# Kernel optimization log

Measured on AMD Instinct MI355X. Metric: run time of the kernel, lower is better.

Reference implementation:

```python
import jax, jax.numpy as jnp
import numpy as np

N_NODES = 50000


def gcn_conv(x, src, dst, W, b):
    """PyG GCNConv: symmetric-normalized aggregation with self-loops.
    out[i] = sum_{j->i} deg^{-1/2}[j] deg^{-1/2}[i] (x_j @ W) + b
    src/dst already include self-loop edges.
    """
    n = x.shape[0]
    ew = jnp.ones(src.shape[0], dtype=x.dtype)
    deg = jax.ops.segment_sum(ew, dst, num_segments=n)  # [N]
    dinv = jnp.where(deg > 0, jax.lax.rsqrt(deg), 0.0).astype(x.dtype)
    norm = dinv[src] * dinv[dst]  # [E+N]
    xw = x @ W  # [N, z] dense transform first (as PyG does)
    msg = xw[src] * norm[:, None]  # gather + scale, [E+N, z]
    out = jax.ops.segment_sum(msg, dst, num_segments=n)  # scatter-add
    return out + b


def prelu(x, a):
    return jnp.where(x > 0, x, a * x)


def setup_inputs() -> dict:
    key = jax.random.key(0)
    k1, k2, k3, k4 = jax.random.split(key, 4)
    in_dim = z_dim = 96
    n_edges = 800000
    x = jax.random.normal(k1, (N_NODES, in_dim), dtype=jnp.float32)
    edge_index = jax.random.randint(k2, (2, n_edges), 0, N_NODES, dtype=jnp.int32)
    # Glorot-style init for GCN weights
    s1 = 1.0 / np.sqrt(in_dim)
    W1 = jax.random.uniform(k3, (in_dim, z_dim), jnp.float32, -s1, s1)
    W2 = jax.random.uniform(k4, (z_dim, z_dim), jnp.float32, -s1, s1)
    b1 = jnp.zeros((z_dim,), jnp.float32)
    b2 = jnp.zeros((z_dim,), jnp.float32)
    prelu_a = jnp.full((z_dim,), 0.25, jnp.float32)  # shared PReLU, per-channel
    return {"x": x, "edge_index": edge_index, "W1": W1, "b1": b1,
            "W2": W2, "b2": b2, "prelu_a": prelu_a}


def reference(x, edge_index, W1, b1, W2, b2, prelu_a):
    n = x.shape[0]
    loop = jnp.arange(n, dtype=edge_index.dtype)
    src = jnp.concatenate([edge_index[0], loop])
    dst = jnp.concatenate([edge_index[1], loop])
    h = prelu(gcn_conv(x, src, dst, W1, b1), prelu_a)
    h = prelu(gcn_conv(h, src, dst, W2, b2), prelu_a)
    return h
```

## Files before the change

### kernel.cpp

```cpp
#include <hip/hip_runtime.h>
#include <hip/hip_fp16.h>

#define D 96
#define D4 24
#define MAXBINS 256

static inline size_t alignup(size_t x) { return (x + 255) & ~size_t(255); }

__device__ inline float4 f4fma(float s, float4 a, float4 acc) {
    acc.x = fmaf(s, a.x, acc.x);
    acc.y = fmaf(s, a.y, acc.y);
    acc.z = fmaf(s, a.z, acc.z);
    acc.w = fmaf(s, a.w, acc.w);
    return acc;
}

__device__ inline void u4add(uint4 rv, float4& a0, float4& a1) {
    __half2 h0 = *reinterpret_cast<__half2*>(&rv.x);
    __half2 h1 = *reinterpret_cast<__half2*>(&rv.y);
    __half2 h2 = *reinterpret_cast<__half2*>(&rv.z);
    __half2 h3 = *reinterpret_cast<__half2*>(&rv.w);
    float2 f0 = __half22float2(h0);
    float2 f1 = __half22float2(h1);
    float2 f2 = __half22float2(h2);
    float2 f3 = __half22float2(h3);
    a0.x += f0.x; a0.y += f0.y; a0.z += f1.x; a0.w += f1.y;
    a1.x += f2.x; a1.y += f2.y; a1.z += f3.x; a1.w += f3.y;
}


__global__ __launch_bounds__(1024) void hist_kernel(const int* __restrict__ dst, int E,
                                                    int* __restrict__ bhist, int nbins) {
    __shared__ int h[MAXBINS];
    const int tid = threadIdx.x;
    if (tid < nbins) h[tid] = 0;
    __syncthreads();
    int e = blockIdx.x * 1024 + tid;
    if (e < E) atomicAdd(&h[dst[e] >> 8], 1);
    __syncthreads();
    if (tid < nbins) bhist[blockIdx.x * nbins + tid] = h[tid];
}

__global__ __launch_bounds__(1024) void scan1_kernel(const int* __restrict__ bhist,
                                                     int* __restrict__ boffs,
                                                     int* __restrict__ bsum,
                                                     int m, int nblk, int nbins) {
    __shared__ int wsum[16];
    const int i = blockIdx.x * 1024 + threadIdx.x;
    const int lane = threadIdx.x & 63;
    const int wid  = threadIdx.x >> 6;
    int v = 0;
    if (i < m) {
        int b = i % nblk, bin = i / nblk;
        v = bhist[b * nbins + bin];
    }
    int sc = v;
    #pragma unroll
    for (int off = 1; off < 64; off <<= 1) {
        int t = __shfl_up(sc, off);
        if (lane >= off) sc += t;
    }
    if (lane == 63) wsum[wid] = sc;
    __syncthreads();
    int wprefix = 0;
    #pragma unroll
    for (int k = 0; k < 16; ++k)
        if (k < wid) wprefix += wsum[k];
    if (i < m) boffs[i] = wprefix + (sc - v);
    if (threadIdx.x == 1023) bsum[blockIdx.x] = wprefix + sc;
}

__global__ __launch_bounds__(1024) void scan2_kernel(const int* __restrict__ bsum,
                                                     int* __restrict__ boff, int nb) {
    __shared__ int wsum[16];
    const int lane = threadIdx.x & 63;
    const int wid  = threadIdx.x >> 6;
    int v = ((int)threadIdx.x < nb) ? bsum[threadIdx.x] : 0;
    int sc = v;
    #pragma unroll
    for (int off = 1; off < 64; off <<= 1) {
        int t = __shfl_up(sc, off);
        if (lane >= off) sc += t;
    }
    if (lane == 63) wsum[wid] = sc;
    __syncthreads();
    int wprefix = 0;
    #pragma unroll
    for (int k = 0; k < 16; ++k)
        if (k < wid) wprefix += wsum[k];
    if ((int)threadIdx.x < nb) boff[threadIdx.x] = wprefix + (sc - v);
}

__global__ __launch_bounds__(1024) void dist_kernel(const int* __restrict__ src,
                                                    const int* __restrict__ dst, int E,
                                                    const int* __restrict__ boffs,
                                                    const int* __restrict__ bboff,
                                                    int nblk, int nbins,
                                                    int* __restrict__ esrc,
                                                    unsigned char* __restrict__ ed8) {
    __shared__ int h[MAXBINS];
    __shared__ int base[MAXBINS];
    const int tid = threadIdx.x;
    if (tid < nbins) h[tid] = 0;
    __syncthreads();
    int e = blockIdx.x * 1024 + tid;
    int s = 0, d = 0, bin = 0, rank = 0;
    bool valid = e < E;
    if (valid) {
        s = src[e]; d = dst[e];
        bin = d >> 8;
        rank = atomicAdd(&h[bin], 1);
    }
    __syncthreads();
    if (tid < nbins) {
        int idx = tid * nblk + blockIdx.x;
        base[tid] = boffs[idx] + bboff[idx >> 10];
    }
    __syncthreads();
    if (valid) {
        int pos = base[bin] + rank;
        esrc[pos] = s;
        ed8[pos] = (unsigned char)(d & 255);
    }
}

__global__ __launch_bounds__(256) void bucketAB_kernel(const int* __restrict__ esrc,
                                                       const unsigned char* __restrict__ ed8,
                                                       const int* __restrict__ boffs,
                                                       const int* __restrict__ bboff,
                                                       int nblk, int nbins,
                                                       float* __restrict__ dinv,
                                                       int* __restrict__ rowptr,
                                                       int* __restrict__ csr,
                                                       int n, int E) {
    __shared__ int cnt[256];
    __shared__ int cur[256];
    __shared__ int wsum[4];
    const int k = blockIdx.x;
    const int tid = threadIdx.x;
    int i0 = k * nblk, i1 = (k + 1) * nblk;
    const int bstart = boffs[i0] + bboff[i0 >> 10];
    const int bend = (k + 1 < nbins) ? (boffs[i1] + bboff[i1 >> 10]) : E;
    cnt[tid] = 0;
    __syncthreads();
    for (int e = bstart + tid; e < bend; e += 256)
        atomicAdd(&cnt[ed8[e]], 1);
    __syncthreads();
    int v = cnt[tid];
    const int lane = tid & 63, wid = tid >> 6;
    int sc = v;
    #pragma unroll
    for (int off = 1; off < 64; off <<= 1) {
        int t = __shfl_up(sc, off);
        if (lane >= off) sc += t;
    }
    if (lane == 63) wsum[wid] = sc;
    __syncthreads();
    int wprefix = 0;
    #pragma unroll
    for (int w = 0; w < 4; ++w)
        if (w < wid) wprefix += wsum[w];
    int mybase = bstart + wprefix + (sc - v);
    int node = k * 256 + tid;
    if (node < n) {
        dinv[node] = rsqrtf((float)(v + 1));
        rowptr[node] = mybase;
    }
    if (k == nbins - 1 && tid == 0) rowptr[n] = E;
    cur[tid] = mybase;
    __syncthreads();
    for (int e = bstart + tid; e < bend; e += 256) {
        int pos = atomicAdd(&cur[ed8[e]], 1);
        csr[pos] = esrc[e];
    }
}


__global__ __launch_bounds__(192) void matmul_kernel(const float* __restrict__ X,
                                                     const float* __restrict__ W,
                                                     const float* __restrict__ dinv,
                                                     uint2* __restrict__ Y, int n) {
    __shared__ float XsT[96 * 64];
    const int t = threadIdx.x;
    const int y = threadIdx.y;
    const int tid = y * 24 + t;
    const int row0 = blockIdx.x * 64;
    const float4* X4 = (const float4*)X;

    for (int i = tid; i < 64 * 24; i += 192) {
        int r = i / 24, c4 = i % 24;
        float4 v = make_float4(0.f, 0.f, 0.f, 0.f);
        if (row0 + r < n) v = X4[(size_t)(row0 + r) * D4 + c4];
        int rs = r ^ ((c4 & 15) << 2);
        XsT[(c4 * 4 + 0) * 64 + rs] = v.x;
        XsT[(c4 * 4 + 1) * 64 + rs] = v.y;
        XsT[(c4 * 4 + 2) * 64 + rs] = v.z;
        XsT[(c4 * 4 + 3) * 64 + rs] = v.w;
    }
    __syncthreads();

    const float4* W4 = (const float4*)W;
    float4 acc[8];
    #pragma unroll
    for (int r = 0; r < 8; ++r) acc[r] = make_float4(0.f, 0.f, 0.f, 0.f);
    const int rbase = y * 8;

    #pragma unroll 8
    for (int k = 0; k < 96; ++k) {
        float4 w = W4[k * D4 + t];
        int base0 = (rbase ^ (((k >> 2) & 15) << 2));
        float4 xa = *(const float4*)&XsT[k * 64 + base0];
        float4 xb = *(const float4*)&XsT[k * 64 + (base0 ^ 4)];
        acc[0] = f4fma(xa.x, w, acc[0]);
        acc[1] = f4fma(xa.y, w, acc[1]);
        acc[2] = f4fma(xa.z, w, acc[2]);
        acc[3] = f4fma(xa.w, w, acc[3]);
        acc[4] = f4fma(xb.x, w, acc[4]);
        acc[5] = f4fma(xb.y, w, acc[5]);
        acc[6] = f4fma(xb.z, w, acc[6]);
        acc[7] = f4fma(xb.w, w, acc[7]);
    }

    #pragma unroll
    for (int r = 0; r < 8; ++r) {
        int row = row0 + rbase + r;
        if (row < n) {
            float sc = dinv[row];
            __half2 ha = __float22half2_rn(make_float2(sc * acc[r].x, sc * acc[r].y));
            __half2 hb = __float22half2_rn(make_float2(sc * acc[r].z, sc * acc[r].w));
            uint2 st;
            st.x = *reinterpret_cast<unsigned int*>(&ha);
            st.y = *reinterpret_cast<unsigned int*>(&hb);
            Y[(size_t)row * D4 + t] = st;
        }
    }
}

__global__ __launch_bounds__(384) void aggregate_kernel(const uint4* __restrict__ XH4,
                                                        const int* __restrict__ csr,
                                                        const int* __restrict__ rowptr,
                                                        const float* __restrict__ dinv,
                                                        const float4* __restrict__ b4,
                                                        const float4* __restrict__ pa4,
                                                        float4* __restrict__ out4, int n) {
    const int i = blockIdx.x * 32 + threadIdx.y;
    const int t = threadIdx.x;
    if (i >= n) return;
    const int beg = rowptr[i], end = rowptr[i + 1];
    float4 a0 = make_float4(0.f, 0.f, 0.f, 0.f);
    float4 a1 = make_float4(0.f, 0.f, 0.f, 0.f);
    int p = beg;
    for (; p + 8 <= end; p += 8) {
        int s0 = csr[p + 0];
        int s1 = csr[p + 1];
        int s2 = csr[p + 2];
        int s3 = csr[p + 3];
        int s4 = csr[p + 4];
        int s5 = csr[p + 5];
        int s6 = csr[p + 6];
        int s7 = csr[p + 7];
        uint4 r0 = XH4[(size_t)s0 * 12 + t];
        uint4 r1 = XH4[(size_t)s1 * 12 + t];
        uint4 r2 = XH4[(size_t)s2 * 12 + t];
        uint4 r3 = XH4[(size_t)s3 * 12 + t];
        uint4 r4 = XH4[(size_t)s4 * 12 + t];
        uint4 r5 = XH4[(size_t)s5 * 12 + t];
        uint4 r6 = XH4[(size_t)s6 * 12 + t];
        uint4 r7 = XH4[(size_t)s7 * 12 + t];
        u4add(r0, a0, a1);
        u4add(r1, a0, a1);
        u4add(r2, a0, a1);
        u4add(r3, a0, a1);
        u4add(r4, a0, a1);
        u4add(r5, a0, a1);
        u4add(r6, a0, a1);
        u4add(r7, a0, a1);
    }
    if (p + 4 <= end) {
        int s0 = csr[p + 0];
        int s1 = csr[p + 1];
        int s2 = csr[p + 2];
        int s3 = csr[p + 3];
        uint4 r0 = XH4[(size_t)s0 * 12 + t];
        uint4 r1 = XH4[(size_t)s1 * 12 + t];
        uint4 r2 = XH4[(size_t)s2 * 12 + t];
        uint4 r3 = XH4[(size_t)s3 * 12 + t];
        u4add(r0, a0, a1);
        u4add(r1, a0, a1);
        u4add(r2, a0, a1);
        u4add(r3, a0, a1);
        p += 4;
    }
    for (; p < end; ++p)
        u4add(XH4[(size_t)csr[p] * 12 + t], a0, a1);
    u4add(XH4[(size_t)i * 12 + t], a0, a1);
    const float di = dinv[i];
    float4 b0 = b4[2 * t], b1 = b4[2 * t + 1];
    float4 q0 = pa4[2 * t], q1 = pa4[2 * t + 1];
    float4 v0, v1;
    v0.x = fmaf(di, a0.x, b0.x);
    v0.y = fmaf(di, a0.y, b0.y);
    v0.z = fmaf(di, a0.z, b0.z);
    v0.w = fmaf(di, a0.w, b0.w);
    v1.x = fmaf(di, a1.x, b1.x);
    v1.y = fmaf(di, a1.y, b1.y);
    v1.z = fmaf(di, a1.z, b1.z);
    v1.w = fmaf(di, a1.w, b1.w);
    v0.x = v0.x > 0.f ? v0.x : q0.x * v0.x;
    v0.y = v0.y > 0.f ? v0.y : q0.y * v0.y;
    v0.z = v0.z > 0.f ? v0.z : q0.z * v0.z;
    v0.w = v0.w > 0.f ? v0.w : q0.w * v0.w;
    v1.x = v1.x > 0.f ? v1.x : q1.x * v1.x;
    v1.y = v1.y > 0.f ? v1.y : q1.y * v1.y;
    v1.z = v1.z > 0.f ? v1.z : q1.z * v1.z;
    v1.w = v1.w > 0.f ? v1.w : q1.w * v1.w;
    out4[(size_t)i * D4 + 2 * t] = v0;
    out4[(size_t)i * D4 + 2 * t + 1] = v1;
}

extern "C" void kernel_launch(void* const* d_in, const int* in_sizes, int n_in,
                              void* d_out, int out_size, void* d_ws, size_t ws_size,
                              hipStream_t stream) {
    const float* x   = (const float*)d_in[0];
    const int*   ei  = (const int*)d_in[1];
    const float* W1  = (const float*)d_in[2];
    const float* b1  = (const float*)d_in[3];
    const float* W2  = (const float*)d_in[4];
    const float* b2  = (const float*)d_in[5];
    const float* pa  = (const float*)d_in[6];
    const int n = in_sizes[0] / D;
    const int E = in_sizes[1] / 2;
    const int* srcp = ei;
    const int* dstp = ei + E;

    const int nbins  = (n + 255) / 256;
    const int nblk_e = (E + 1023) / 1024;
    const int m      = nbins * nblk_e;
    const int nbscan = (m + 1023) / 1024;

    char* w = (char*)d_ws;
    int*   bhist  = (int*)w;   w += alignup((size_t)m * 4);
    int*   boffs  = (int*)w;   w += alignup((size_t)m * 4);
    int*   bsum   = (int*)w;   w += alignup(1024 * 4);
    int*   bboff  = (int*)w;   w += alignup(1024 * 4);
    float* dinv   = (float*)w; w += alignup((size_t)n * 4);
    int*   rowptr = (int*)w;   w += alignup((size_t)(n + 1) * 4);
    int*   esrc   = (int*)w;   w += alignup((size_t)E * 4);
    unsigned char* ed8 = (unsigned char*)w;  w += alignup((size_t)E);
    int*   csr    = (int*)w;   w += alignup((size_t)E * 4);
    uint4* xw     = (uint4*)w; w += alignup((size_t)n * D * 2);
    float* out    = (float*)d_out;

    hist_kernel<<<nblk_e, 1024, 0, stream>>>(dstp, E, bhist, nbins);
    scan1_kernel<<<nbscan, 1024, 0, stream>>>(bhist, boffs, bsum, m, nblk_e, nbins);
    scan2_kernel<<<1, 1024, 0, stream>>>(bsum, bboff, nbscan);
    dist_kernel<<<nblk_e, 1024, 0, stream>>>(srcp, dstp, E, boffs, bboff, nblk_e, nbins,
                                             esrc, ed8);
    bucketAB_kernel<<<nbins, 256, 0, stream>>>(esrc, ed8, boffs, bboff, nblk_e, nbins,
                                               dinv, rowptr, csr, n, E);

    dim3 mblk(24, 8);
    const int mgrid = (n + 63) / 64;
    dim3 ablk(12, 32);
    const int agrid = (n + 31) / 32;

    matmul_kernel<<<mgrid, mblk, 0, stream>>>(x, W1, dinv, (uint2*)xw, n);
    aggregate_kernel<<<agrid, ablk, 0, stream>>>(xw, csr, rowptr, dinv,
                                                 (const float4*)b1, (const float4*)pa, (float4*)out, n);
    matmul_kernel<<<mgrid, mblk, 0, stream>>>(out, W2, dinv, (uint2*)xw, n);
    aggregate_kernel<<<agrid, ablk, 0, stream>>>(xw, csr, rowptr, dinv,
                                                 (const float4*)b2, (const float4*)pa, (float4*)out, n);
}
```

Before: 153.5 us.

## Degree-sort nodes within bins for aggregation and store hidden layer in fp16

The bucket kernel now builds a per-bin permutation that sorts nodes by in-degree (capped at 63), so each aggregation block processes nodes with similar edge counts and warp divergence from uneven loop lengths is reduced. The intermediate hidden activations between the two GCN layers are written in fp16 instead of fp32, and the second matmul reads them back in half precision, roughly halving that round-trip traffic. This costs an extra perm array and indirection, scattered output writes, and some added rounding error in the hidden layer.

```diff
diff --git a/kernel.cpp b/kernel.cpp
--- a/kernel.cpp
+++ b/kernel.cpp
@@ -26,6 +26,32 @@
     float2 f3 = __half22float2(h3);
     a0.x += f0.x; a0.y += f0.y; a0.z += f1.x; a0.w += f1.y;
     a1.x += f2.x; a1.y += f2.y; a1.z += f3.x; a1.w += f3.y;
+}
+
+__device__ inline uint4 pack8(float4 v0, float4 v1) {
+    __half2 h0 = __float22half2_rn(make_float2(v0.x, v0.y));
+    __half2 h1 = __float22half2_rn(make_float2(v0.z, v0.w));
+    __half2 h2 = __float22half2_rn(make_float2(v1.x, v1.y));
+    __half2 h3 = __float22half2_rn(make_float2(v1.z, v1.w));
+    uint4 r;
+    r.x = *reinterpret_cast<unsigned int*>(&h0);
+    r.y = *reinterpret_cast<unsigned int*>(&h1);
+    r.z = *reinterpret_cast<unsigned int*>(&h2);
+    r.w = *reinterpret_cast<unsigned int*>(&h3);
+    return r;
+}
+
+__device__ inline void unpack8(uint4 rv, float* f) {
+    __half2 h0 = *reinterpret_cast<__half2*>(&rv.x);
+    __half2 h1 = *reinterpret_cast<__half2*>(&rv.y);
+    __half2 h2 = *reinterpret_cast<__half2*>(&rv.z);
+    __half2 h3 = *reinterpret_cast<__half2*>(&rv.w);
+    float2 f0 = __half22float2(h0);
+    float2 f1 = __half22float2(h1);
+    float2 f2 = __half22float2(h2);
+    float2 f3 = __half22float2(h3);
+    f[0] = f0.x; f[1] = f0.y; f[2] = f1.x; f[3] = f1.y;
+    f[4] = f2.x; f[5] = f2.y; f[6] = f3.x; f[7] = f3.y;
 }
 
 
@@ -132,16 +158,20 @@
                                                        float* __restrict__ dinv,
                                                        int* __restrict__ rowptr,
                                                        int* __restrict__ csr,
+                                                       int* __restrict__ perm,
                                                        int n, int E) {
     __shared__ int cnt[256];
     __shared__ int cur[256];
     __shared__ int wsum[4];
+    __shared__ int dh[64];
+    __shared__ int dbase[64];
     const int k = blockIdx.x;
     const int tid = threadIdx.x;
     int i0 = k * nblk, i1 = (k + 1) * nblk;
     const int bstart = boffs[i0] + bboff[i0 >> 10];
     const int bend = (k + 1 < nbins) ? (boffs[i1] + bboff[i1 >> 10]) : E;
     cnt[tid] = 0;
+    if (tid < 64) dh[tid] = 0;
     __syncthreads();
     for (int e = bstart + tid; e < bend; e += 256)
         atomicAdd(&cnt[ed8[e]], 1);
@@ -155,20 +185,36 @@
         if (lane >= off) sc += t;
     }
     if (lane == 63) wsum[wid] = sc;
+    int node = k * 256 + tid;
+    int dbin = v < 63 ? v : 63;
+    if (node < n) atomicAdd(&dh[dbin], 1);
     __syncthreads();
     int wprefix = 0;
     #pragma unroll
     for (int w = 0; w < 4; ++w)
         if (w < wid) wprefix += wsum[w];
     int mybase = bstart + wprefix + (sc - v);
-    int node = k * 256 + tid;
     if (node < n) {
         dinv[node] = rsqrtf((float)(v + 1));
         rowptr[node] = mybase;
     }
     if (k == nbins - 1 && tid == 0) rowptr[n] = E;
     cur[tid] = mybase;
-    __syncthreads();
+    if (tid < 64) {
+        int vv = dh[tid];
+        int s2 = vv;
+        #pragma unroll
+        for (int off = 1; off < 64; off <<= 1) {
+            int t2 = __shfl_up(s2, off);
+            if (tid >= off) s2 += t2;
+        }
+        dbase[tid] = s2 - vv;
+    }
+    __syncthreads();
+    if (node < n) {
+        int pos = atomicAdd(&dbase[dbin], 1);
+        perm[k * 256 + pos] = node;
+    }
     for (int e = bstart + tid; e < bend; e += 256) {
         int pos = atomicAdd(&cur[ed8[e]], 1);
         csr[pos] = esrc[e];
@@ -176,7 +222,8 @@
 }
 
 
-__global__ __launch_bounds__(192) void matmul_kernel(const float* __restrict__ X,
+template<int IN16>
+__global__ __launch_bounds__(192) void matmul_kernel(const void* __restrict__ Xv,
                                                      const float* __restrict__ W,
                                                      const float* __restrict__ dinv,
                                                      uint2* __restrict__ Y, int n) {
@@ -185,17 +232,39 @@
     const int y = threadIdx.y;
     const int tid = y * 24 + t;
     const int row0 = blockIdx.x * 64;
-    const float4* X4 = (const float4*)X;
-
-    for (int i = tid; i < 64 * 24; i += 192) {
-        int r = i / 24, c4 = i % 24;
-        float4 v = make_float4(0.f, 0.f, 0.f, 0.f);
-        if (row0 + r < n) v = X4[(size_t)(row0 + r) * D4 + c4];
-        int rs = r ^ ((c4 & 15) << 2);
-        XsT[(c4 * 4 + 0) * 64 + rs] = v.x;
-        XsT[(c4 * 4 + 1) * 64 + rs] = v.y;
-        XsT[(c4 * 4 + 2) * 64 + rs] = v.z;
-        XsT[(c4 * 4 + 3) * 64 + rs] = v.w;
+
+    if (IN16) {
+        const uint4* XH = (const uint4*)Xv;
+        for (int i = tid; i < 64 * 12; i += 192) {
+            int r = i / 12, c8 = i % 12;
+            uint4 v = make_uint4(0u, 0u, 0u, 0u);
+            if (row0 + r < n) v = XH[(size_t)(row0 + r) * 12 + c8];
+            float f[8];
+            unpack8(v, f);
+            int c4a = 2 * c8, c4b = 2 * c8 + 1;
+            int rsa = r ^ ((c4a & 15) << 2);
+            int rsb = r ^ ((c4b & 15) << 2);
+            XsT[(c4a * 4 + 0) * 64 + rsa] = f[0];
+            XsT[(c4a * 4 + 1) * 64 + rsa] = f[1];
+            XsT[(c4a * 4 + 2) * 64 + rsa] = f[2];
+            XsT[(c4a * 4 + 3) * 64 + rsa] = f[3];
+            XsT[(c4b * 4 + 0) * 64 + rsb] = f[4];
+            XsT[(c4b * 4 + 1) * 64 + rsb] = f[5];
+            XsT[(c4b * 4 + 2) * 64 + rsb] = f[6];
+            XsT[(c4b * 4 + 3) * 64 + rsb] = f[7];
+        }
+    } else {
+        const float4* X4 = (const float4*)Xv;
+        for (int i = tid; i < 64 * 24; i += 192) {
+            int r = i / 24, c4 = i % 24;
+            float4 v = make_float4(0.f, 0.f, 0.f, 0.f);
+            if (row0 + r < n) v = X4[(size_t)(row0 + r) * D4 + c4];
+            int rs = r ^ ((c4 & 15) << 2);
+            XsT[(c4 * 4 + 0) * 64 + rs] = v.x;
+            XsT[(c4 * 4 + 1) * 64 + rs] = v.y;
+            XsT[(c4 * 4 + 2) * 64 + rs] = v.z;
+            XsT[(c4 * 4 + 3) * 64 + rs] = v.w;
+        }
     }
     __syncthreads();
 
@@ -236,16 +305,19 @@
     }
 }
 
+template<int OUT16>
 __global__ __launch_bounds__(384) void aggregate_kernel(const uint4* __restrict__ XH4,
                                                         const int* __restrict__ csr,
                                                         const int* __restrict__ rowptr,
                                                         const float* __restrict__ dinv,
+                                                        const int* __restrict__ perm,
                                                         const float4* __restrict__ b4,
                                                         const float4* __restrict__ pa4,
-                                                        float4* __restrict__ out4, int n) {
-    const int i = blockIdx.x * 32 + threadIdx.y;
+                                                        void* __restrict__ outv, int n) {
+    const int j = blockIdx.x * 32 + threadIdx.y;
     const int t = threadIdx.x;
-    if (i >= n) return;
+    if (j >= n) return;
+    const int i = perm[j];
     const int beg = rowptr[i], end = rowptr[i + 1];
     float4 a0 = make_float4(0.f, 0.f, 0.f, 0.f);
     float4 a1 = make_float4(0.f, 0.f, 0.f, 0.f);
@@ -314,8 +386,13 @@
     v1.y = v1.y > 0.f ? v1.y : q1.y * v1.y;
     v1.z = v1.z > 0.f ? v1.z : q1.z * v1.z;
     v1.w = v1.w > 0.f ? v1.w : q1.w * v1.w;
-    out4[(size_t)i * D4 + 2 * t] = v0;
-    out4[(size_t)i * D4 + 2 * t + 1] = v1;
+    if (OUT16) {
+        ((uint4*)outv)[(size_t)i * 12 + t] = pack8(v0, v1);
+    } else {
+        float4* out4 = (float4*)outv;
+        out4[(size_t)i * D4 + 2 * t] = v0;
+        out4[(size_t)i * D4 + 2 * t + 1] = v1;
+    }
 }
 
 extern "C" void kernel_launch(void* const* d_in, const int* in_sizes, int n_in,
@@ -345,10 +422,12 @@
     int*   bboff  = (int*)w;   w += alignup(1024 * 4);
     float* dinv   = (float*)w; w += alignup((size_t)n * 4);
     int*   rowptr = (int*)w;   w += alignup((size_t)(n + 1) * 4);
+    int*   perm   = (int*)w;   w += alignup((size_t)n * 4);
     int*   esrc   = (int*)w;   w += alignup((size_t)E * 4);
     unsigned char* ed8 = (unsigned char*)w;  w += alignup((size_t)E);
     int*   csr    = (int*)w;   w += alignup((size_t)E * 4);
     uint4* xw     = (uint4*)w; w += alignup((size_t)n * D * 2);
+    uint4* h16    = (uint4*)w; w += alignup((size_t)n * D * 2);
     float* out    = (float*)d_out;
 
     hist_kernel<<<nblk_e, 1024, 0, stream>>>(dstp, E, bhist, nbins);
@@ -357,17 +436,17 @@
     dist_kernel<<<nblk_e, 1024, 0, stream>>>(srcp, dstp, E, boffs, bboff, nblk_e, nbins,
                                              esrc, ed8);
     bucketAB_kernel<<<nbins, 256, 0, stream>>>(esrc, ed8, boffs, bboff, nblk_e, nbins,
-                                               dinv, rowptr, csr, n, E);
+                                               dinv, rowptr, csr, perm, n, E);
 
     dim3 mblk(24, 8);
     const int mgrid = (n + 63) / 64;
     dim3 ablk(12, 32);
     const int agrid = (n + 31) / 32;
 
-    matmul_kernel<<<mgrid, mblk, 0, stream>>>(x, W1, dinv, (uint2*)xw, n);
-    aggregate_kernel<<<agrid, ablk, 0, stream>>>(xw, csr, rowptr, dinv,
-                                                 (const float4*)b1, (const float4*)pa, (float4*)out, n);
-    matmul_kernel<<<mgrid, mblk, 0, stream>>>(out, W2, dinv, (uint2*)xw, n);
-    aggregate_kernel<<<agrid, ablk, 0, stream>>>(xw, csr, rowptr, dinv,
-                                                 (const float4*)b2, (const float4*)pa, (float4*)out, n);
-}
+    matmul_kernel<0><<<mgrid, mblk, 0, stream>>>(x, W1, dinv, (uint2*)xw, n);
+    aggregate_kernel<1><<<agrid, ablk, 0, stream>>>(xw, csr, rowptr, dinv, perm,
+                                                    (const float4*)b1, (const float4*)pa, h16, n);
+    matmul_kernel<1><<<mgrid, mblk, 0, stream>>>(h16, W2, dinv, (uint2*)xw, n);
+    aggregate_kernel<0><<<agrid, ablk, 0, stream>>>(xw, csr, rowptr, dinv, perm,
+                                                    (const float4*)b2, (const float4*)pa, out, n);
+}
```

After: 158.6 us. +3.3%, slower.
